# Optimization experiments

Measured on AMD Instinct MI355X. Metric: run time of the kernel, lower is better.

Reference implementation:

```python
import math
import numpy as np
import jax
import jax.numpy as jnp

RANK = 8
KITER = 2
EPS = 1e-5


def frft_time(z, alpha):
    # z: complex64 [B, T, C]; fractional Fourier transform along axis 1
    # via Bluestein-style chirp multiplication + FFT convolution.
    T = z.shape[1]
    a = (float(alpha) + math.pi) % (2.0 * math.pi) - math.pi
    if abs(a) < 1e-6:
        return z
    if abs(abs(a) - math.pi) < 1e-6:
        ph = np.complex64(np.exp(1j * math.copysign(math.pi / 2, a)))
        return ph * jnp.flip(z, axis=1)
    sa = math.sin(a)
    s = math.copysign(1.0 / max(1e-7, abs(sa)), sa)
    c = math.cos(a) / max(1e-7, sa)
    t = np.linspace(-1.0, 1.0, T)
    dt = 2.0 / (T - 1)
    tail = (1,) * (z.ndim - 2)
    pre = jnp.asarray(np.exp(1j * np.pi * (c + s) * t ** 2).astype(np.complex64)).reshape(1, T, *tail)
    g = z * pre
    m = np.arange(-(T - 1), T)
    L = 1 << (2 * T - 2).bit_length()  # next pow2 >= 2T-1
    h_pad = np.zeros(L, np.complex64)
    h_pad[m % L] = np.exp(-1j * np.pi * s * (m * dt) ** 2).astype(np.complex64)
    H = jnp.asarray(np.fft.fft(h_pad).astype(np.complex64)).reshape(1, L, *tail)
    pad = [(0, 0), (0, L - T)] + [(0, 0)] * (z.ndim - 2)
    G = jnp.fft.fft(jnp.pad(g, pad), axis=1)
    conv = jnp.fft.ifft(G * H, axis=1)[:, T - 1:T - 1 + T]
    pref = np.complex64(np.sqrt(np.complex64(1.0 - 1j * c)))
    return pref * pre * conv * np.float32(dt)


def _orthonorm(V):
    # batched reduced QR with deterministic column signs (sign of diag(R))
    Q, R = jnp.linalg.qr(V)
    d = jnp.diagonal(R, axis1=-2, axis2=-1)
    return Q * jnp.sign(d + EPS)[:, None, :]


def _forward(x, Win_shift, Wout_shift, b_shift, W_out, ln_gamma, ln_beta):
    B, T, D = x.shape
    anchor = jnp.zeros((B, D), x.dtype).at[:, 0].set(1.0)
    xc = x - anchor[:, None, :]
    # LowRankShift: S(x) = W_out_shift @ gelu(W_in_shift @ x) + b
    s = jax.nn.gelu(x @ Win_shift.T, approximate=False) @ Wout_shift.T + b_shift
    xprime = xc + s
    xpc = xprime.astype(jnp.complex64)
    alphas = np.linspace(0.15, 2.99, RANK)
    # per-alpha FrFT-domain energy weights
    weights = []
    for alpha in alphas:
        X_a = frft_time(xpc, alpha)
        E_a = jnp.mean(jnp.abs(X_a) ** 2, axis=2)  # [B,T]
        w_a = jnp.sqrt(E_a + 1e-6)  # pow p=0.5
        w_a = w_a / (jnp.mean(w_a, axis=1, keepdims=True) + 1e-6)
        weights.append((float(alpha), w_a))

    def Komega(Y):  # Y: real [B,T,r]
        Yc = Y.astype(jnp.complex64)
        acc = 0.0
        for alpha, w in weights:
            Ya = frft_time(Yc, alpha)
            acc = acc + frft_time(w[..., None].astype(jnp.complex64) * Ya, -alpha)
        return (acc / len(weights)).real

    # subspace iteration with identity init
    E0 = jnp.zeros((B, D, RANK), x.dtype).at[:, :RANK, :].set(jnp.eye(RANK, dtype=x.dtype))
    V = _orthonorm(E0)
    for _ in range(KITER):
        Y = Komega(xprime @ V)  # [B,T,r]
        Z = jnp.einsum('btd,btr->bdr', xprime, Y) / float(T)
        V = _orthonorm(Z + EPS * V)
    # sign-align columns to anchor
    sgn = jnp.sign(jnp.sum(V * anchor[:, :, None], axis=1) + 1e-12)
    V = V * sgn[:, None, :]
    traces = xprime @ V  # [B,T,r]
    scales = jnp.sqrt(jnp.sum(traces ** 2, axis=1, keepdims=True) + EPS)
    traces_n = traces / scales
    # shrink_lambda == 0 -> soft_shrink identity; SpiralMix(rank=1) has no pairs -> identity
    traces_final = traces_n * scales
    x_tilde = jnp.einsum('btr,bdr->btd', traces_final, V)
    x_hat = x_tilde - s + anchor[:, None, :]
    y = x + x_hat @ W_out.T  # dropout eval mode
    mu = jnp.mean(y, axis=-1, keepdims=True)
    var = jnp.mean((y - mu) ** 2, axis=-1, keepdims=True)
    return (y - mu) / jnp.sqrt(var + 1e-5) * ln_gamma + ln_beta


def setup_inputs():
    key = jax.random.key(0)
    k = jax.random.split(key, 5)
    B, T, D, SR = 4, 2048, 256, 128
    return {
        'x': jax.random.normal(k[0], (B, T, D), jnp.float32),
        'Win_shift': jax.random.normal(k[1], (SR, D), jnp.float32) / np.float32(np.sqrt(D)),
        'Wout_shift': jax.random.normal(k[2], (D, SR), jnp.float32) / np.float32(np.sqrt(SR)),
        'b_shift': jax.random.normal(k[3], (D,), jnp.float32) * 0.01,
        'W_out': jax.random.normal(k[4], (D, D), jnp.float32) / np.float32(np.sqrt(D)),
        'ln_gamma': jnp.ones((D,), jnp.float32),
        'ln_beta': jnp.zeros((D,), jnp.float32),
    }


def reference(x, Win_shift, Wout_shift, b_shift, W_out, ln_gamma, ln_beta):
    return _forward(x, Win_shift, Wout_shift, b_shift, W_out, ln_gamma, ln_beta)
```

## Files before the change

### kernel.cpp

```cpp
#include <hip/hip_runtime.h>
#include <math.h>

#define Bb 4
#define Tt 2048
#define Dd 256
#define SRr 128
#define Rr 8
#define NA 8
#define NV 16
#define Lf 4096
#define EPSf 1e-5f
#define PI_D 3.14159265358979323846

#define OFF_TW4R  0
#define OFF_TW4I  (OFF_TW4R + 4096)
#define OFF_PRER  (OFF_TW4I + 4096)
#define OFF_PREI  (OFF_PRER + NV*Tt)
#define OFF_POSR  (OFF_PREI + NV*Tt)
#define OFF_POSI  (OFF_POSR + NV*Tt)
#define OFF_PM2   (OFF_POSI + NV*Tt)
#define OFF_H     (OFF_PM2 + NA*Tt)
#define OFF_WINT  (OFF_H + NV*Lf*2)
#define OFF_WOUTT (OFF_WINT + Dd*SRr)
#define OFF_WOT   (OFF_WOUTT + SRr*Dd)
#define OFF_WTAB  (OFF_WOT + Dd*Dd)
#define OFF_ESUM  (OFF_WTAB + NA*Bb*Tt)
#define OFF_V     (OFF_ESUM + NA*Bb*Tt)
#define OFF_M     (OFF_V + Bb*Dd*Rr)
#define OFF_YT    (OFF_M + Bb*Dd*Rr)
#define OFF_YACC  (OFF_YT + Bb*Rr*Tt)
#define OFF_S     (OFF_YACC + Bb*Rr*Tt)
#define OFF_XPT   (OFF_S + Bb*Tt*Dd)

__device__ __forceinline__ float block_reduce_sum(float v, float* red, int tid){
  #pragma unroll
  for (int o = 32; o > 0; o >>= 1) v += __shfl_xor(v, o, 64);
  __syncthreads();
  if ((tid & 63) == 0) red[tid >> 6] = v;
  __syncthreads();
  return red[0] + red[1] + red[2] + red[3];
}

__device__ void variant_params(int v, double& s_, double& c_){
  double step = (2.99 - 0.15) / 7.0;
  int idx = v & 7;
  double alpha = (idx == 7) ? 2.99 : (0.15 + (double)idx * step);
  if (v >= 8) alpha = -alpha;
  double a = fmod(alpha + PI_D, 2.0 * PI_D);
  if (a < 0.0) a += 2.0 * PI_D;
  a -= PI_D;
  double sa = sin(a);
  s_ = ((sa >= 0.0) ? 1.0 : -1.0) / fmax(1e-7, fabs(sa));
  c_ = cos(a) / fmax(1e-7, sa);
}

struct cpx { float r, i; };
__device__ __forceinline__ cpx cmul(cpx a, cpx b){ return {a.r*b.r - a.i*b.i, a.r*b.i + a.i*b.r}; }
__device__ __forceinline__ cpx cmulj(cpx a, cpx b){ return {a.r*b.r + a.i*b.i, a.i*b.r - a.r*b.i}; }

__device__ __forceinline__ void fft4(cpx& a, cpx& b, cpx& c, cpx& d, float sgn){
  cpx t0{a.r+c.r, a.i+c.i}, t1{a.r-c.r, a.i-c.i};
  cpx t2{b.r+d.r, b.i+d.i}, t3{b.r-d.r, b.i-d.i};
  a = {t0.r+t2.r, t0.i+t2.i};
  c = {t0.r-t2.r, t0.i-t2.i};
  b = {t1.r - sgn*t3.i, t1.i + sgn*t3.r};
  d = {t1.r + sgn*t3.i, t1.i - sgn*t3.r};
}

__device__ __forceinline__ void fft16(cpx x[16], float sgn){
  const float WC[10] = {1.f, 0.92387953251128674f, 0.70710678118654752f, 0.38268343236508977f,
                        0.f, -0.38268343236508977f, -0.70710678118654752f, -0.92387953251128674f,
                        -1.f, -0.92387953251128674f};
  const float WS[10] = {0.f, 0.38268343236508977f, 0.70710678118654752f, 0.92387953251128674f,
                        1.f, 0.92387953251128674f, 0.70710678118654752f, 0.38268343236508977f,
                        0.f, -0.38268343236508977f};
  #pragma unroll
  for (int j0 = 0; j0 < 4; ++j0)
    fft4(x[j0], x[j0+4], x[j0+8], x[j0+12], sgn);
  #pragma unroll
  for (int j0 = 1; j0 < 4; ++j0){
    #pragma unroll
    for (int p0 = 1; p0 < 4; ++p0){
      int m = j0*p0;
      cpx w{WC[m], sgn*WS[m]};
      x[j0 + 4*p0] = cmul(x[j0 + 4*p0], w);
    }
  }
  #pragma unroll
  for (int p0 = 0; p0 < 4; ++p0)
    fft4(x[4*p0+0], x[4*p0+1], x[4*p0+2], x[4*p0+3], sgn);
  cpx t;
  t=x[1];  x[1]=x[4];   x[4]=t;
  t=x[2];  x[2]=x[8];   x[8]=t;
  t=x[3];  x[3]=x[12];  x[12]=t;
  t=x[6];  x[6]=x[9];   x[9]=t;
  t=x[7];  x[7]=x[13];  x[13]=t;
  t=x[11]; x[11]=x[14]; x[14]=t;
}

__device__ __forceinline__ void fft4096(cpx x[16], float* sre, float* sim,
                                        const cpx twA[16], const cpx twB[16],
                                        int tid, float sgn){
  int hi = tid >> 4, lo = tid & 15;
  fft16(x, sgn);
  #pragma unroll
  for (int p = 1; p < 16; ++p) x[p] = (sgn < 0.f) ? cmul(x[p], twA[p]) : cmulj(x[p], twA[p]);
  __syncthreads();
  #pragma unroll
  for (int p = 0; p < 16; ++p){ int a = p*272 + 17*hi + lo; sre[a] = x[p].r; sim[a] = x[p].i; }
  __syncthreads();
  #pragma unroll
  for (int u = 0; u < 16; ++u){ int a = hi*272 + 17*u + lo; x[u] = {sre[a], sim[a]}; }
  fft16(x, sgn);
  #pragma unroll
  for (int q = 1; q < 16; ++q) x[q] = (sgn < 0.f) ? cmul(x[q], twB[q]) : cmulj(x[q], twB[q]);
  __syncthreads();
  #pragma unroll
  for (int q = 0; q < 16; ++q){ int a = hi*272 + 17*q + lo; sre[a] = x[q].r; sim[a] = x[q].i; }
  __syncthreads();
  #pragma unroll
  for (int v = 0; v < 16; ++v){ int a = hi*272 + 17*lo + v; x[v] = {sre[a], sim[a]}; }
  fft16(x, sgn);
}

__global__ void k_twiddle(float* ws){
  int id = blockIdx.x*256 + threadIdx.x;
  for (int k = id; k < 4096; k += 4096){
    double ang = -2.0 * PI_D * (double)k / (double)Lf;
    ws[OFF_TW4R + k] = (float)cos(ang);
    ws[OFF_TW4I + k] = (float)sin(ang);
  }
}

__global__ void k_tables(float* ws){
  int v = blockIdx.x;
  double s_, c_;
  variant_params(v, s_, c_);
  double dt = 2.0 / (double)(Tt - 1);
  double cf = (double)(float)c_;
  double rmag = sqrt(1.0 + cf * cf);
  double pr = sqrt((rmag + 1.0) * 0.5);
  double pim = ((cf >= 0.0) ? -1.0 : 1.0) * sqrt(fmax(0.0, (rmag - 1.0) * 0.5));
  double cps = PI_D * (c_ + s_);
  double sc = dt / (double)Lf;
  for (int k = threadIdx.x; k < Tt; k += 256){
    double t = (k == Tt - 1) ? 1.0 : ((double)k * dt - 1.0);
    double th = cps * (t * t);
    double cr = cos(th), ci = sin(th);
    ws[OFF_PRER + v*Tt + k] = (float)cr;
    ws[OFF_PREI + v*Tt + k] = (float)ci;
    float por = (float)((pr*cr - pim*ci) * sc);
    float poi = (float)((pr*ci + pim*cr) * sc);
    ws[OFF_POSR + v*Tt + k] = por;
    ws[OFF_POSI + v*Tt + k] = poi;
    if (v < NA) ws[OFF_PM2 + v*Tt + k] = por*por + poi*poi;
  }
}

__global__ __launch_bounds__(256) void k_hfft(float* ws){
  __shared__ float sre[16*272], sim[16*272];
  int v = blockIdx.x, tid = threadIdx.x;
  int hi = tid >> 4, lo = tid & 15;
  int base = hi + 16*lo;
  double s_, c_;
  variant_params(v, s_, c_);
  double dt = 2.0 / (double)(Tt - 1);
  double ns = -(PI_D * s_);
  const float* tw4r = ws + OFF_TW4R; const float* tw4i = ws + OFF_TW4I;
  cpx twA[16], twB[16];
  #pragma unroll
  for (int p = 0; p < 16; ++p){
    int iA = tid * p;      twA[p] = {tw4r[iA], tw4i[iA]};
    int iB = 16 * lo * p;  twB[p] = {tw4r[iB], tw4i[iB]};
  }
  cpx x[16];
  #pragma unroll
  for (int j = 0; j < 16; ++j){
    int n = j*256 + tid;
    if (n == 2048){ x[j] = {0.f, 0.f}; continue; }
    int m = (n <= 2047) ? n : (n - 4096);
    double md = (double)m * dt;
    double th = ns * (md * md);
    x[j] = {(float)cos(th), (float)sin(th)};
  }
  fft4096(x, sre, sim, twA, twB, tid, -1.f);
  #pragma unroll
  for (int r = 0; r < 16; ++r){
    int k = base + 256*r;
    ws[OFF_H + (v*Lf + k)*2 + 0] = x[r].r;
    ws[OFF_H + (v*Lf + k)*2 + 1] = x[r].i;
  }
}

__global__ void k_transpose(const float* Win, const float* Wout, const float* Wo, float* ws){
  int id = blockIdx.x * 256 + threadIdx.x;
  { int d = id & (Dd-1); int k = id >> 8; ws[OFF_WOT + id] = Wo[d*Dd + k]; }
  if (id < Dd*SRr){
    int c = id & (SRr-1); int k = id >> 7;
    ws[OFF_WINT + id] = Win[c*Dd + k];
    int d2 = id & (Dd-1); int k2 = id >> 8;
    ws[OFF_WOUTT + id] = Wout[d2*SRr + k2];
  }
}

__global__ __launch_bounds__(256) void k_shift(const float* x, const float* bsh, float* ws){
  __shared__ float xs[16][Dd];
  __shared__ float us[16][SRr];
  int tid = threadIdx.x;
  int g0 = blockIdx.x * 16;
  int b = g0 >> 11, t0 = g0 & (Tt - 1);
  #pragma unroll
  for (int row = 0; row < 16; ++row)
    xs[row][tid] = x[(g0 + row)*Dd + tid];
  __syncthreads();
  int col = tid & 127, rowgrp = tid >> 7;
  {
    float acc[8];
    #pragma unroll
    for (int rr = 0; rr < 8; ++rr) acc[rr] = 0.f;
    const float* WT = ws + OFF_WINT;
    for (int k = 0; k < Dd; ++k){
      float w = WT[k*SRr + col];
      #pragma unroll
      for (int rr = 0; rr < 8; ++rr)
        acc[rr] = fmaf(xs[rowgrp*8 + rr][k], w, acc[rr]);
    }
    #pragma unroll
    for (int rr = 0; rr < 8; ++rr){
      float a = acc[rr];
      us[rowgrp*8 + rr][col] = 0.5f * a * (1.0f + erff(a * 0.70710678118654752f));
    }
  }
  __syncthreads();
  float sacc[16];
  float bv = bsh[tid];
  #pragma unroll
  for (int row = 0; row < 16; ++row) sacc[row] = bv;
  const float* WT2 = ws + OFF_WOUTT;
  for (int k = 0; k < SRr; ++k){
    float w = WT2[k*Dd + tid];
    #pragma unroll
    for (int row = 0; row < 16; ++row)
      sacc[row] = fmaf(us[row][k], w, sacc[row]);
  }
  float xp[16];
  #pragma unroll
  for (int row = 0; row < 16; ++row){
    float xv = xs[row][tid];
    float anc = (tid == 0) ? 1.0f : 0.0f;
    ws[OFF_S + (g0 + row)*Dd + tid] = sacc[row];
    xp[row] = xv - anc + sacc[row];
  }
  float* xpt = ws + OFF_XPT + (b*Dd + tid)*Tt + t0;
  #pragma unroll
  for (int q = 0; q < 4; ++q)
    *reinterpret_cast<float4*>(xpt + 4*q) = make_float4(xp[4*q], xp[4*q+1], xp[4*q+2], xp[4*q+3]);
}

__global__ __launch_bounds__(256) void k_weights(float* ws){
  __shared__ float sre[16*272], sim[16*272];
  int tid = threadIdx.x;
  int chunk = blockIdx.x, b = blockIdx.y, z = blockIdx.z;
  int hi = tid >> 4, lo = tid & 15;
  int base = hi + 16*lo;
  const float* tw4r = ws + OFF_TW4R; const float* tw4i = ws + OFF_TW4I;
  cpx twA[16], twB[16];
  #pragma unroll
  for (int p = 0; p < 16; ++p){
    int iA = tid * p;      twA[p] = {tw4r[iA], tw4i[iA]};
    int iB = 16 * lo * p;  twB[p] = {tw4r[iB], tw4i[iB]};
  }
  const float* prer = ws + OFF_PRER + z*Tt;
  const float* prei = ws + OFF_PREI + z*Tt;
  const float* pm2  = ws + OFF_PM2  + z*Tt;
  const float* Hv   = ws + OFF_H    + z*Lf*2;
  float e[16];
  #pragma unroll
  for (int r = 0; r < 16; ++r) e[r] = 0.f;
  for (int cc = 0; cc < 8; ++cc){
    int c = chunk*8 + cc;
    const float* xcol = ws + OFF_XPT + (b*Dd + c)*Tt;
    cpx x[16];
    #pragma unroll
    for (int j = 0; j < 16; ++j){
      if (j < 8){
        int t = j*256 + tid;
        float xv = xcol[t];
        x[j] = {xv * prer[t], xv * prei[t]};
      } else x[j] = {0.f, 0.f};
    }
    fft4096(x, sre, sim, twA, twB, tid, -1.f);
    #pragma unroll
    for (int r = 0; r < 16; ++r){
      int k = base + 256*r;
      cpx h{Hv[2*k], Hv[2*k+1]};
      x[r] = cmul(x[r], h);
    }
    __syncthreads();
    #pragma unroll
    for (int r = 0; r < 16; ++r){ int a = r*272 + 17*lo + hi; sre[a] = x[r].r; sim[a] = x[r].i; }
    __syncthreads();
    #pragma unroll
    for (int j = 0; j < 16; ++j){ int a = j*272 + 17*hi + lo; x[j] = {sre[a], sim[a]}; }
    fft4096(x, sre, sim, twA, twB, tid, +1.f);
    #pragma unroll
    for (int r = 0; r < 16; ++r){
      int k = base + 256*r;
      if (k >= 2047 && k < 4095){
        int t = k - 2047;
        e[r] += pm2[t] * (x[r].r*x[r].r + x[r].i*x[r].i);
      }
    }
  }
  float* Ez = ws + OFF_ESUM + (z*Bb + b)*Tt;
  #pragma unroll
  for (int r = 0; r < 16; ++r){
    int k = base + 256*r;
    if (k >= 2047 && k < 4095) atomicAdd(&Ez[k - 2047], e[r]);
  }
}

__global__ void k_wnorm(float* ws){
  __shared__ float red[4];
  int b = blockIdx.x, z = blockIdx.y, tid = threadIdx.x;
  const float* Ez = ws + OFF_ESUM + (z*Bb + b)*Tt;
  float* wz = ws + OFF_WTAB + (z*Bb + b)*Tt;
  float wr[8]; float psum = 0.f;
  #pragma unroll
  for (int k = 0; k < 8; ++k){
    float Ea = Ez[tid + k*256] * (1.0f / (float)Dd);
    wr[k] = sqrtf(Ea + 1e-6f);
    psum += wr[k];
  }
  float tot = block_reduce_sum(psum, red, tid);
  float inv = 1.0f / (tot / (float)Tt + 1e-6f);
  #pragma unroll
  for (int k = 0; k < 8; ++k) wz[tid + k*256] = wr[k] * inv;
}

__global__ void k_vinit(float* ws){
  int id = blockIdx.x*256 + threadIdx.x;
  int r = id & (Rr-1); int d = (id >> 3) & (Dd-1);
  ws[OFF_V + id] = (d == r) ? 1.f : 0.f;
}

__global__ void k_traces(float* ws){
  __shared__ float Vl[Dd*Rr];
  int tile = blockIdx.x, b = blockIdx.y, tid = threadIdx.x;
  for (int i = tid; i < Dd*Rr; i += 256) Vl[i] = ws[OFF_V + b*Dd*Rr + i];
  __syncthreads();
  int t = tile*256 + tid;
  float acc[Rr];
  #pragma unroll
  for (int r = 0; r < Rr; ++r) acc[r] = 0.f;
  const float* xp = ws + OFF_XPT + (b*Dd)*Tt + t;
  for (int d = 0; d < Dd; ++d){
    float xv = xp[d*Tt];
    #pragma unroll
    for (int r = 0; r < Rr; ++r) acc[r] = fmaf(xv, Vl[d*Rr + r], acc[r]);
  }
  #pragma unroll
  for (int r = 0; r < Rr; ++r) ws[OFF_YT + (b*Rr + r)*Tt + t] = acc[r];
}

__global__ __launch_bounds__(256) void k_komega(float* ws){
  __shared__ float sre[16*272], sim[16*272];
  int tid = threadIdx.x;
  int rr = blockIdx.x, b = blockIdx.y, z = blockIdx.z;
  int hi = tid >> 4, lo = tid & 15;
  int base = hi + 16*lo;
  int v1 = z, v2 = z + NA;
  const float* tw4r = ws + OFF_TW4R; const float* tw4i = ws + OFF_TW4I;
  cpx twA[16], twB[16];
  #pragma unroll
  for (int p = 0; p < 16; ++p){
    int iA = tid * p;      twA[p] = {tw4r[iA], tw4i[iA]};
    int iB = 16 * lo * p;  twB[p] = {tw4r[iB], tw4i[iB]};
  }
  const float* prer1 = ws + OFF_PRER + v1*Tt; const float* prei1 = ws + OFF_PREI + v1*Tt;
  const float* posr1 = ws + OFF_POSR + v1*Tt; const float* posi1 = ws + OFF_POSI + v1*Tt;
  const float* prer2 = ws + OFF_PRER + v2*Tt; const float* prei2 = ws + OFF_PREI + v2*Tt;
  const float* posr2 = ws + OFF_POSR + v2*Tt; const float* posi2 = ws + OFF_POSI + v2*Tt;
  const float* H1 = ws + OFF_H + v1*Lf*2;
  const float* H2 = ws + OFF_H + v2*Lf*2;
  const float* wz = ws + OFF_WTAB + (z*Bb + b)*Tt;
  const float* ycol = ws + OFF_YT + (b*Rr + rr)*Tt;
  float* yac = ws + OFF_YACC + (b*Rr + rr)*Tt;
  cpx x[16];
  #pragma unroll
  for (int j = 0; j < 16; ++j){
    if (j < 8){
      int t = j*256 + tid;
      float yv = ycol[t];
      x[j] = {yv * prer1[t], yv * prei1[t]};
    } else x[j] = {0.f, 0.f};
  }
  fft4096(x, sre, sim, twA, twB, tid, -1.f);
  #pragma unroll
  for (int r = 0; r < 16; ++r){ int k = base + 256*r; cpx h{H1[2*k], H1[2*k+1]}; x[r] = cmul(x[r], h); }
  __syncthreads();
  #pragma unroll
  for (int r = 0; r < 16; ++r){ int a = r*272 + 17*lo + hi; sre[a] = x[r].r; sim[a] = x[r].i; }
  __syncthreads();
  #pragma unroll
  for (int j = 0; j < 16; ++j){ int a = j*272 + 17*hi + lo; x[j] = {sre[a], sim[a]}; }
  fft4096(x, sre, sim, twA, twB, tid, +1.f);
  __syncthreads();
  #pragma unroll
  for (int r = 0; r < 16; ++r){
    int k = base + 256*r;
    if (k >= 2047 && k < 4095){
      int t = k - 2047;
      float cr = x[r].r, ci = x[r].i;
      float wv = wz[t];
      float yar = (posr1[t]*cr - posi1[t]*ci) * wv;
      float yai = (posr1[t]*ci + posi1[t]*cr) * wv;
      float gr = yar*prer2[t] - yai*prei2[t];
      float gi = yar*prei2[t] + yai*prer2[t];
      int a = (t >> 8)*272 + 17*((t >> 4) & 15) + (t & 15);
      sre[a] = gr; sim[a] = gi;
    }
  }
  __syncthreads();
  #pragma unroll
  for (int j = 0; j < 16; ++j){
    if (j < 8){ int a = j*272 + 17*hi + lo; x[j] = {sre[a], sim[a]}; }
    else x[j] = {0.f, 0.f};
  }
  fft4096(x, sre, sim, twA, twB, tid, -1.f);
  #pragma unroll
  for (int r = 0; r < 16; ++r){ int k = base + 256*r; cpx h{H2[2*k], H2[2*k+1]}; x[r] = cmul(x[r], h); }
  __syncthreads();
  #pragma unroll
  for (int r = 0; r < 16; ++r){ int a = r*272 + 17*lo + hi; sre[a] = x[r].r; sim[a] = x[r].i; }
  __syncthreads();
  #pragma unroll
  for (int j = 0; j < 16; ++j){ int a = j*272 + 17*hi + lo; x[j] = {sre[a], sim[a]}; }
  fft4096(x, sre, sim, twA, twB, tid, +1.f);
  #pragma unroll
  for (int r = 0; r < 16; ++r){
    int k = base + 256*r;
    if (k >= 2047 && k < 4095){
      int t = k - 2047;
      atomicAdd(&yac[t], posr2[t]*x[r].r - posi2[t]*x[r].i);
    }
  }
}

__global__ void k_zm(float* ws){
  __shared__ float red[4];
  int d = blockIdx.x, b = blockIdx.y, tid = threadIdx.x;
  const float* xcol = ws + OFF_XPT + (b*Dd + d)*Tt;
  for (int r = 0; r < Rr; ++r){
    const float* ycol = ws + OFF_YACC + (b*Rr + r)*Tt;
    float p = 0.f;
    for (int t = tid; t < Tt; t += 256) p = fmaf(xcol[t], ycol[t], p);
    float tot = block_reduce_sum(p, red, tid);
    if (tid == 0){
      float zval = tot / (float)(Tt * NA);
      ws[OFF_M + (b*Dd + d)*Rr + r] = zval + EPSf * ws[OFF_V + (b*Dd + d)*Rr + r];
    }
  }
}

__global__ void k_mgs(float* ws){
  __shared__ float q[Rr][Dd];
  __shared__ float red[4];
  int b = blockIdx.x, tid = threadIdx.x;
  float m[Rr];
  #pragma unroll
  for (int r = 0; r < Rr; ++r) m[r] = ws[OFF_M + (b*Dd + tid)*Rr + r];
  for (int r = 0; r < Rr; ++r){
    float v = m[r];
    for (int j = 0; j < r; ++j){
      float dotv = block_reduce_sum(q[j][tid] * v, red, tid);
      v = fmaf(-dotv, q[j][tid], v);
    }
    float n2 = block_reduce_sum(v * v, red, tid);
    q[r][tid] = v / sqrtf(n2);
    __syncthreads();
  }
  #pragma unroll
  for (int r = 0; r < Rr; ++r) ws[OFF_V + (b*Dd + tid)*Rr + r] = q[r][tid];
}

__global__ __launch_bounds__(256) void k_out(const float* x, const float* g, const float* be,
                                             float* ws, float* out){
  __shared__ float hs[16][Dd + 1];
  __shared__ float ytl[16][Rr];
  __shared__ float mv_mu[16], mv_rs[16];
  int tid = threadIdx.x;
  int g0 = blockIdx.x * 16;
  int b = g0 >> 11, t0 = g0 & (Tt - 1);
  if (tid < 128){
    int row = tid >> 3, r = tid & 7;
    ytl[row][r] = ws[OFF_YT + (b*Rr + r)*Tt + t0 + row];
  }
  float vr[Rr];
  {
    const float4* Vb = reinterpret_cast<const float4*>(ws + OFF_V + (b*Dd + tid)*Rr);
    float4 v0 = Vb[0], v1 = Vb[1];
    vr[0]=v0.x; vr[1]=v0.y; vr[2]=v0.z; vr[3]=v0.w;
    vr[4]=v1.x; vr[5]=v1.y; vr[6]=v1.z; vr[7]=v1.w;
  }
  __syncthreads();
  #pragma unroll
  for (int row = 0; row < 16; ++row){
    float acc = 0.f;
    #pragma unroll
    for (int r = 0; r < Rr; ++r) acc = fmaf(ytl[row][r], vr[r], acc);
    acc -= ws[OFF_S + (g0 + row)*Dd + tid];
    if (tid == 0) acc += 1.0f;
    hs[row][tid] = acc;
  }
  __syncthreads();
  float acc[16];
  #pragma unroll
  for (int row = 0; row < 16; ++row) acc[row] = x[(g0 + row)*Dd + tid];
  const float* WT = ws + OFF_WOT;
  for (int k = 0; k < Dd; ++k){
    float w = WT[k*Dd + tid];
    #pragma unroll
    for (int row = 0; row < 16; ++row)
      acc[row] = fmaf(hs[row][k], w, acc[row]);
  }
  __syncthreads();
  #pragma unroll
  for (int row = 0; row < 16; ++row) hs[row][tid] = acc[row];
  __syncthreads();
  {
    int row = tid >> 4, j = tid & 15;
    float yv[16]; float sum = 0.f;
    #pragma unroll
    for (int mth = 0; mth < 16; ++mth){ yv[mth] = hs[row][j + 16*mth]; sum += yv[mth]; }
    #pragma unroll
    for (int o = 8; o > 0; o >>= 1) sum += __shfl_xor(sum, o, 16);
    float mu = sum * (1.0f / (float)Dd);
    float ssq = 0.f;
    #pragma unroll
    for (int mth = 0; mth < 16; ++mth){ float d = yv[mth] - mu; ssq = fmaf(d, d, ssq); }
    #pragma unroll
    for (int o = 8; o > 0; o >>= 1) ssq += __shfl_xor(ssq, o, 16);
    if (j == 0){ mv_mu[row] = mu; mv_rs[row] = rsqrtf(ssq * (1.0f / (float)Dd) + 1e-5f); }
  }
  __syncthreads();
  float gg = g[tid], bb = be[tid];
  #pragma unroll
  for (int row = 0; row < 16; ++row)
    out[(g0 + row)*Dd + tid] = (acc[row] - mv_mu[row]) * mv_rs[row] * gg + bb;
}

extern "C" void kernel_launch(void* const* d_in, const int* in_sizes, int n_in,
                              void* d_out, int out_size, void* d_ws, size_t ws_size,
                              hipStream_t stream){
  (void)in_sizes; (void)n_in; (void)out_size; (void)ws_size;
  const float* x    = (const float*)d_in[0];
  const float* Win  = (const float*)d_in[1];
  const float* Wout = (const float*)d_in[2];
  const float* bsh  = (const float*)d_in[3];
  const float* Wo   = (const float*)d_in[4];
  const float* g    = (const float*)d_in[5];
  const float* be   = (const float*)d_in[6];
  float* ws  = (float*)d_ws;
  float* out = (float*)d_out;

  hipLaunchKernelGGL(k_twiddle, dim3(16), dim3(256), 0, stream, ws);
  hipLaunchKernelGGL(k_tables, dim3(NV), dim3(256), 0, stream, ws);
  hipLaunchKernelGGL(k_hfft, dim3(NV), dim3(256), 0, stream, ws);
  hipLaunchKernelGGL(k_transpose, dim3(Dd*Dd/256), dim3(256), 0, stream, Win, Wout, Wo, ws);
  hipLaunchKernelGGL(k_shift, dim3(Bb*Tt/16), dim3(256), 0, stream, x, bsh, ws);
  hipMemsetAsync(ws + OFF_ESUM, 0, (size_t)NA*Bb*Tt*sizeof(float), stream);
  hipLaunchKernelGGL(k_weights, dim3(Dd/8, Bb, NA), dim3(256), 0, stream, ws);
  hipLaunchKernelGGL(k_wnorm, dim3(Bb, NA), dim3(256), 0, stream, ws);
  hipLaunchKernelGGL(k_vinit, dim3(Bb*Dd*Rr/256), dim3(256), 0, stream, ws);
  for (int it = 0; it < 2; ++it){
    hipLaunchKernelGGL(k_traces, dim3(Tt/256, Bb), dim3(256), 0, stream, ws);
    hipMemsetAsync(ws + OFF_YACC, 0, (size_t)Bb*Rr*Tt*sizeof(float), stream);
    hipLaunchKernelGGL(k_komega, dim3(Rr, Bb, NA), dim3(256), 0, stream, ws);
    hipLaunchKernelGGL(k_zm, dim3(Dd, Bb), dim3(256), 0, stream, ws);
    hipLaunchKernelGGL(k_mgs, dim3(Bb), dim3(256), 0, stream, ws);
  }
  hipLaunchKernelGGL(k_traces, dim3(Tt/256, Bb), dim3(256), 0, stream, ws);
  hipLaunchKernelGGL(k_out, dim3(Bb*Tt/16), dim3(256), 0, stream, x, g, be, ws, out);
}
```

Before: 487.6 us.

## Merge setup kernels, skip zero-padded FFT stage, replace atomics with per-alpha buffers

```diff
diff --git a/kernel.cpp b/kernel.cpp
--- a/kernel.cpp
+++ b/kernel.cpp
@@ -28,8 +28,8 @@
 #define OFF_V     (OFF_ESUM + NA*Bb*Tt)
 #define OFF_M     (OFF_V + Bb*Dd*Rr)
 #define OFF_YT    (OFF_M + Bb*Dd*Rr)
-#define OFF_YACC  (OFF_YT + Bb*Rr*Tt)
-#define OFF_S     (OFF_YACC + Bb*Rr*Tt)
+#define OFF_YAC8  (OFF_YT + Bb*Rr*Tt)
+#define OFF_S     (OFF_YAC8 + NA*Bb*Rr*Tt)
 #define OFF_XPT   (OFF_S + Bb*Tt*Dd)
 
 __device__ __forceinline__ float block_reduce_sum(float v, float* red, int tid){
@@ -67,6 +67,7 @@
   d = {t1.r + sgn*t3.i, t1.i - sgn*t3.r};
 }
 
+template<int ZP>
 __device__ __forceinline__ void fft16(cpx x[16], float sgn){
   const float WC[10] = {1.f, 0.92387953251128674f, 0.70710678118654752f, 0.38268343236508977f,
                         0.f, -0.38268343236508977f, -0.70710678118654752f, -0.92387953251128674f,
@@ -74,9 +75,20 @@
   const float WS[10] = {0.f, 0.38268343236508977f, 0.70710678118654752f, 0.92387953251128674f,
                         1.f, 0.92387953251128674f, 0.70710678118654752f, 0.38268343236508977f,
                         0.f, -0.38268343236508977f};
-  #pragma unroll
-  for (int j0 = 0; j0 < 4; ++j0)
-    fft4(x[j0], x[j0+4], x[j0+8], x[j0+12], sgn);
+  if (ZP){
+    #pragma unroll
+    for (int j0 = 0; j0 < 4; ++j0){
+      cpx a = x[j0], b = x[j0+4];
+      x[j0]    = {a.r + b.r,       a.i + b.i};
+      x[j0+4]  = {a.r - sgn*b.i,   a.i + sgn*b.r};
+      x[j0+8]  = {a.r - b.r,       a.i - b.i};
+      x[j0+12] = {a.r + sgn*b.i,   a.i - sgn*b.r};
+    }
+  } else {
+    #pragma unroll
+    for (int j0 = 0; j0 < 4; ++j0)
+      fft4(x[j0], x[j0+4], x[j0+8], x[j0+12], sgn);
+  }
   #pragma unroll
   for (int j0 = 1; j0 < 4; ++j0){
     #pragma unroll
@@ -98,81 +110,85 @@
   t=x[11]; x[11]=x[14]; x[14]=t;
 }
 
-__device__ __forceinline__ void fft4096(cpx x[16], float* sre, float* sim,
-                                        const cpx twA[16], const cpx twB[16],
-                                        int tid, float sgn){
+template<int ZP>
+__device__ __forceinline__ void fft4096c(cpx x[16], float2* sh,
+                                         const cpx twA[16], const cpx twB[16],
+                                         int tid, float sgn){
   int hi = tid >> 4, lo = tid & 15;
-  fft16(x, sgn);
+  fft16<ZP>(x, sgn);
   #pragma unroll
   for (int p = 1; p < 16; ++p) x[p] = (sgn < 0.f) ? cmul(x[p], twA[p]) : cmulj(x[p], twA[p]);
   __syncthreads();
   #pragma unroll
-  for (int p = 0; p < 16; ++p){ int a = p*272 + 17*hi + lo; sre[a] = x[p].r; sim[a] = x[p].i; }
-  __syncthreads();
-  #pragma unroll
-  for (int u = 0; u < 16; ++u){ int a = hi*272 + 17*u + lo; x[u] = {sre[a], sim[a]}; }
-  fft16(x, sgn);
+  for (int p = 0; p < 16; ++p){ sh[p*272 + 17*hi + lo] = make_float2(x[p].r, x[p].i); }
+  __syncthreads();
+  #pragma unroll
+  for (int u = 0; u < 16; ++u){ float2 v = sh[hi*272 + 17*u + lo]; x[u] = {v.x, v.y}; }
+  fft16<0>(x, sgn);
   #pragma unroll
   for (int q = 1; q < 16; ++q) x[q] = (sgn < 0.f) ? cmul(x[q], twB[q]) : cmulj(x[q], twB[q]);
   __syncthreads();
   #pragma unroll
-  for (int q = 0; q < 16; ++q){ int a = hi*272 + 17*q + lo; sre[a] = x[q].r; sim[a] = x[q].i; }
-  __syncthreads();
-  #pragma unroll
-  for (int v = 0; v < 16; ++v){ int a = hi*272 + 17*lo + v; x[v] = {sre[a], sim[a]}; }
-  fft16(x, sgn);
-}
-
-__global__ void k_twiddle(float* ws){
-  int id = blockIdx.x*256 + threadIdx.x;
-  for (int k = id; k < 4096; k += 4096){
-    double ang = -2.0 * PI_D * (double)k / (double)Lf;
-    ws[OFF_TW4R + k] = (float)cos(ang);
-    ws[OFF_TW4I + k] = (float)sin(ang);
-  }
-}
-
-__global__ void k_tables(float* ws){
-  int v = blockIdx.x;
+  for (int q = 0; q < 16; ++q){ sh[hi*272 + 17*q + lo] = make_float2(x[q].r, x[q].i); }
+  __syncthreads();
+  #pragma unroll
+  for (int v = 0; v < 16; ++v){ float2 t = sh[hi*272 + 17*lo + v]; x[v] = {t.x, t.y}; }
+  fft16<0>(x, sgn);
+}
+
+__global__ __launch_bounds__(256) void k_setup(const float* Win, const float* Wout,
+                                               const float* Wo, float* ws){
+  __shared__ float2 sh[16*272];
+  int blk = blockIdx.x, tid = threadIdx.x;
+  int id = blk*256 + tid;
+  { int d = id & (Dd-1); int k = id >> 8; ws[OFF_WOT + id] = Wo[d*Dd + k]; }
+  if (id < Dd*SRr){
+    int c = id & (SRr-1); int k = id >> 7;
+    ws[OFF_WINT + id] = Win[c*Dd + k];
+    int d2 = id & (Dd-1); int k2 = id >> 8;
+    ws[OFF_WOUTT + id] = Wout[d2*SRr + k2];
+  }
+  if (id < 4096){
+    double ang = -2.0 * PI_D * (double)id / (double)Lf;
+    ws[OFF_TW4R + id] = (float)cos(ang);
+    ws[OFF_TW4I + id] = (float)sin(ang);
+  }
+  if (blk >= NV) return;
+  int v = blk;
   double s_, c_;
   variant_params(v, s_, c_);
   double dt = 2.0 / (double)(Tt - 1);
-  double cf = (double)(float)c_;
-  double rmag = sqrt(1.0 + cf * cf);
-  double pr = sqrt((rmag + 1.0) * 0.5);
-  double pim = ((cf >= 0.0) ? -1.0 : 1.0) * sqrt(fmax(0.0, (rmag - 1.0) * 0.5));
-  double cps = PI_D * (c_ + s_);
-  double sc = dt / (double)Lf;
-  for (int k = threadIdx.x; k < Tt; k += 256){
-    double t = (k == Tt - 1) ? 1.0 : ((double)k * dt - 1.0);
-    double th = cps * (t * t);
-    double cr = cos(th), ci = sin(th);
-    ws[OFF_PRER + v*Tt + k] = (float)cr;
-    ws[OFF_PREI + v*Tt + k] = (float)ci;
-    float por = (float)((pr*cr - pim*ci) * sc);
-    float poi = (float)((pr*ci + pim*cr) * sc);
-    ws[OFF_POSR + v*Tt + k] = por;
-    ws[OFF_POSI + v*Tt + k] = poi;
-    if (v < NA) ws[OFF_PM2 + v*Tt + k] = por*por + poi*poi;
-  }
-}
-
-__global__ __launch_bounds__(256) void k_hfft(float* ws){
-  __shared__ float sre[16*272], sim[16*272];
-  int v = blockIdx.x, tid = threadIdx.x;
+  {
+    double cf = (double)(float)c_;
+    double rmag = sqrt(1.0 + cf * cf);
+    double pr = sqrt((rmag + 1.0) * 0.5);
+    double pim = ((cf >= 0.0) ? -1.0 : 1.0) * sqrt(fmax(0.0, (rmag - 1.0) * 0.5));
+    double cps = PI_D * (c_ + s_);
+    double sc = dt / (double)Lf;
+    for (int k = tid; k < Tt; k += 256){
+      double t = (k == Tt - 1) ? 1.0 : ((double)k * dt - 1.0);
+      double th = cps * (t * t);
+      double cr = cos(th), ci = sin(th);
+      ws[OFF_PRER + v*Tt + k] = (float)cr;
+      ws[OFF_PREI + v*Tt + k] = (float)ci;
+      float por = (float)((pr*cr - pim*ci) * sc);
+      float poi = (float)((pr*ci + pim*cr) * sc);
+      ws[OFF_POSR + v*Tt + k] = por;
+      ws[OFF_POSI + v*Tt + k] = poi;
+      if (v < NA) ws[OFF_PM2 + v*Tt + k] = por*por + poi*poi;
+    }
+  }
   int hi = tid >> 4, lo = tid & 15;
   int base = hi + 16*lo;
-  double s_, c_;
-  variant_params(v, s_, c_);
-  double dt = 2.0 / (double)(Tt - 1);
+  cpx twA[16], twB[16];
+  #pragma unroll
+  for (int p = 0; p < 16; ++p){
+    double aA = -2.0 * PI_D * (double)((tid * p) & 4095) / (double)Lf;
+    double aB = -2.0 * PI_D * (double)((16 * lo * p) & 4095) / (double)Lf;
+    twA[p] = {(float)cos(aA), (float)sin(aA)};
+    twB[p] = {(float)cos(aB), (float)sin(aB)};
+  }
   double ns = -(PI_D * s_);
-  const float* tw4r = ws + OFF_TW4R; const float* tw4i = ws + OFF_TW4I;
-  cpx twA[16], twB[16];
-  #pragma unroll
-  for (int p = 0; p < 16; ++p){
-    int iA = tid * p;      twA[p] = {tw4r[iA], tw4i[iA]};
-    int iB = 16 * lo * p;  twB[p] = {tw4r[iB], tw4i[iB]};
-  }
   cpx x[16];
   #pragma unroll
   for (int j = 0; j < 16; ++j){
@@ -183,23 +199,12 @@
     double th = ns * (md * md);
     x[j] = {(float)cos(th), (float)sin(th)};
   }
-  fft4096(x, sre, sim, twA, twB, tid, -1.f);
+  fft4096c<0>(x, sh, twA, twB, tid, -1.f);
   #pragma unroll
   for (int r = 0; r < 16; ++r){
     int k = base + 256*r;
     ws[OFF_H + (v*Lf + k)*2 + 0] = x[r].r;
     ws[OFF_H + (v*Lf + k)*2 + 1] = x[r].i;
-  }
-}
-
-__global__ void k_transpose(const float* Win, const float* Wout, const float* Wo, float* ws){
-  int id = blockIdx.x * 256 + threadIdx.x;
-  { int d = id & (Dd-1); int k = id >> 8; ws[OFF_WOT + id] = Wo[d*Dd + k]; }
-  if (id < Dd*SRr){
-    int c = id & (SRr-1); int k = id >> 7;
-    ws[OFF_WINT + id] = Win[c*Dd + k];
-    int d2 = id & (Dd-1); int k2 = id >> 8;
-    ws[OFF_WOUTT + id] = Wout[d2*SRr + k2];
   }
 }
 
@@ -251,14 +256,14 @@
     ws[OFF_S + (g0 + row)*Dd + tid] = sacc[row];
     xp[row] = xv - anc + sacc[row];
   }
-  float* xpt = ws + OFF_XPT + (b*Dd + tid)*Tt + t0;
+  float* xpt = ws + OFF_XPT + ((size_t)(b*Dd + tid))*Tt + t0;
   #pragma unroll
   for (int q = 0; q < 4; ++q)
     *reinterpret_cast<float4*>(xpt + 4*q) = make_float4(xp[4*q], xp[4*q+1], xp[4*q+2], xp[4*q+3]);
 }
 
-__global__ __launch_bounds__(256) void k_weights(float* ws){
-  __shared__ float sre[16*272], sim[16*272];
+__global__ __launch_bounds__(256, 4) void k_weights(float* ws){
+  __shared__ float2 sh[16*272];
   int tid = threadIdx.x;
   int chunk = blockIdx.x, b = blockIdx.y, z = blockIdx.z;
   int hi = tid >> 4, lo = tid & 15;
@@ -279,17 +284,17 @@
   for (int r = 0; r < 16; ++r) e[r] = 0.f;
   for (int cc = 0; cc < 8; ++cc){
     int c = chunk*8 + cc;
-    const float* xcol = ws + OFF_XPT + (b*Dd + c)*Tt;
+    const float* xcol = ws + OFF_XPT + ((size_t)(b*Dd + c))*Tt;
     cpx x[16];
     #pragma unroll
-    for (int j = 0; j < 16; ++j){
-      if (j < 8){
-        int t = j*256 + tid;
-        float xv = xcol[t];
-        x[j] = {xv * prer[t], xv * prei[t]};
-      } else x[j] = {0.f, 0.f};
-    }
-    fft4096(x, sre, sim, twA, twB, tid, -1.f);
+    for (int j = 0; j < 8; ++j){
+      int t = j*256 + tid;
+      float xv = xcol[t];
+      x[j] = {xv * prer[t], xv * prei[t]};
+    }
+    #pragma unroll
+    for (int j = 8; j < 16; ++j) x[j] = {0.f, 0.f};
+    fft4096c<1>(x, sh, twA, twB, tid, -1.f);
     #pragma unroll
     for (int r = 0; r < 16; ++r){
       int k = base + 256*r;
@@ -298,11 +303,11 @@
     }
     __syncthreads();
     #pragma unroll
-    for (int r = 0; r < 16; ++r){ int a = r*272 + 17*lo + hi; sre[a] = x[r].r; sim[a] = x[r].i; }
+    for (int r = 0; r < 16; ++r){ sh[r*272 + 17*lo + hi] = make_float2(x[r].r, x[r].i); }
     __syncthreads();
     #pragma unroll
-    for (int j = 0; j < 16; ++j){ int a = j*272 + 17*hi + lo; x[j] = {sre[a], sim[a]}; }
-    fft4096(x, sre, sim, twA, twB, tid, +1.f);
+    for (int j = 0; j < 16; ++j){ float2 v = sh[j*272 + 17*hi + lo]; x[j] = {v.x, v.y}; }
+    fft4096c<0>(x, sh, twA, twB, tid, +1.f);
     #pragma unroll
     for (int r = 0; r < 16; ++r){
       int k = base + 256*r;
@@ -338,12 +343,6 @@
   for (int k = 0; k < 8; ++k) wz[tid + k*256] = wr[k] * inv;
 }
 
-__global__ void k_vinit(float* ws){
-  int id = blockIdx.x*256 + threadIdx.x;
-  int r = id & (Rr-1); int d = (id >> 3) & (Dd-1);
-  ws[OFF_V + id] = (d == r) ? 1.f : 0.f;
-}
-
 __global__ void k_traces(float* ws){
   __shared__ float Vl[Dd*Rr];
   int tile = blockIdx.x, b = blockIdx.y, tid = threadIdx.x;
@@ -353,9 +352,9 @@
   float acc[Rr];
   #pragma unroll
   for (int r = 0; r < Rr; ++r) acc[r] = 0.f;
-  const float* xp = ws + OFF_XPT + (b*Dd)*Tt + t;
+  const float* xp = ws + OFF_XPT + ((size_t)(b*Dd))*Tt + t;
   for (int d = 0; d < Dd; ++d){
-    float xv = xp[d*Tt];
+    float xv = xp[(size_t)d*Tt];
     #pragma unroll
     for (int r = 0; r < Rr; ++r) acc[r] = fmaf(xv, Vl[d*Rr + r], acc[r]);
   }
@@ -363,8 +362,8 @@
   for (int r = 0; r < Rr; ++r) ws[OFF_YT + (b*Rr + r)*Tt + t] = acc[r];
 }
 
-__global__ __launch_bounds__(256) void k_komega(float* ws){
-  __shared__ float sre[16*272], sim[16*272];
+__global__ __launch_bounds__(256, 4) void k_komega(float* ws, int useXPT){
+  __shared__ float2 sh[16*272];
   int tid = threadIdx.x;
   int rr = blockIdx.x, b = blockIdx.y, z = blockIdx.z;
   int hi = tid >> 4, lo = tid & 15;
@@ -384,27 +383,28 @@
   const float* H1 = ws + OFF_H + v1*Lf*2;
   const float* H2 = ws + OFF_H + v2*Lf*2;
   const float* wz = ws + OFF_WTAB + (z*Bb + b)*Tt;
-  const float* ycol = ws + OFF_YT + (b*Rr + rr)*Tt;
-  float* yac = ws + OFF_YACC + (b*Rr + rr)*Tt;
+  const float* ycol = useXPT ? (ws + OFF_XPT + ((size_t)(b*Dd + rr))*Tt)
+                             : (ws + OFF_YT + ((size_t)(b*Rr + rr))*Tt);
+  float* yac = ws + OFF_YAC8 + ((size_t)((z*Bb + b)*Rr + rr))*Tt;
   cpx x[16];
   #pragma unroll
-  for (int j = 0; j < 16; ++j){
-    if (j < 8){
-      int t = j*256 + tid;
-      float yv = ycol[t];
-      x[j] = {yv * prer1[t], yv * prei1[t]};
-    } else x[j] = {0.f, 0.f};
-  }
-  fft4096(x, sre, sim, twA, twB, tid, -1.f);
+  for (int j = 0; j < 8; ++j){
+    int t = j*256 + tid;
+    float yv = ycol[t];
+    x[j] = {yv * prer1[t], yv * prei1[t]};
+  }
+  #pragma unroll
+  for (int j = 8; j < 16; ++j) x[j] = {0.f, 0.f};
+  fft4096c<1>(x, sh, twA, twB, tid, -1.f);
   #pragma unroll
   for (int r = 0; r < 16; ++r){ int k = base + 256*r; cpx h{H1[2*k], H1[2*k+1]}; x[r] = cmul(x[r], h); }
   __syncthreads();
   #pragma unroll
-  for (int r = 0; r < 16; ++r){ int a = r*272 + 17*lo + hi; sre[a] = x[r].r; sim[a] = x[r].i; }
-  __syncthreads();
-  #pragma unroll
-  for (int j = 0; j < 16; ++j){ int a = j*272 + 17*hi + lo; x[j] = {sre[a], sim[a]}; }
-  fft4096(x, sre, sim, twA, twB, tid, +1.f);
+  for (int r = 0; r < 16; ++r){ sh[r*272 + 17*lo + hi] = make_float2(x[r].r, x[r].i); }
+  __syncthreads();
+  #pragma unroll
+  for (int j = 0; j < 16; ++j){ float2 v = sh[j*272 + 17*hi + lo]; x[j] = {v.x, v.y}; }
+  fft4096c<0>(x, sh, twA, twB, tid, +1.f);
   __syncthreads();
   #pragma unroll
   for (int r = 0; r < 16; ++r){
@@ -418,47 +418,58 @@
       float gr = yar*prer2[t] - yai*prei2[t];
       float gi = yar*prei2[t] + yai*prer2[t];
       int a = (t >> 8)*272 + 17*((t >> 4) & 15) + (t & 15);
-      sre[a] = gr; sim[a] = gi;
-    }
-  }
-  __syncthreads();
-  #pragma unroll
-  for (int j = 0; j < 16; ++j){
-    if (j < 8){ int a = j*272 + 17*hi + lo; x[j] = {sre[a], sim[a]}; }
-    else x[j] = {0.f, 0.f};
-  }
-  fft4096(x, sre, sim, twA, twB, tid, -1.f);
+      sh[a] = make_float2(gr, gi);
+    }
+  }
+  __syncthreads();
+  #pragma unroll
+  for (int j = 0; j < 8; ++j){ float2 v = sh[j*272 + 17*hi + lo]; x[j] = {v.x, v.y}; }
+  #pragma unroll
+  for (int j = 8; j < 16; ++j) x[j] = {0.f, 0.f};
+  fft4096c<1>(x, sh, twA, twB, tid, -1.f);
   #pragma unroll
   for (int r = 0; r < 16; ++r){ int k = base + 256*r; cpx h{H2[2*k], H2[2*k+1]}; x[r] = cmul(x[r], h); }
   __syncthreads();
   #pragma unroll
-  for (int r = 0; r < 16; ++r){ int a = r*272 + 17*lo + hi; sre[a] = x[r].r; sim[a] = x[r].i; }
-  __syncthreads();
-  #pragma unroll
-  for (int j = 0; j < 16; ++j){ int a = j*272 + 17*hi + lo; x[j] = {sre[a], sim[a]}; }
-  fft4096(x, sre, sim, twA, twB, tid, +1.f);
+  for (int r = 0; r < 16; ++r){ sh[r*272 + 17*lo + hi] = make_float2(x[r].r, x[r].i); }
+  __syncthreads();
+  #pragma unroll
+  for (int j = 0; j < 16; ++j){ float2 v = sh[j*272 + 17*hi + lo]; x[j] = {v.x, v.y}; }
+  fft4096c<0>(x, sh, twA, twB, tid, +1.f);
   #pragma unroll
   for (int r = 0; r < 16; ++r){
     int k = base + 256*r;
     if (k >= 2047 && k < 4095){
       int t = k - 2047;
-      atomicAdd(&yac[t], posr2[t]*x[r].r - posi2[t]*x[r].i);
-    }
-  }
-}
-
-__global__ void k_zm(float* ws){
+      yac[t] = posr2[t]*x[r].r - posi2[t]*x[r].i;
+    }
+  }
+}
+
+__global__ void k_ysum(float* ws){
+  int i = (blockIdx.x*256 + threadIdx.x) * 4;
+  float4 acc = make_float4(0.f, 0.f, 0.f, 0.f);
+  #pragma unroll
+  for (int z = 0; z < NA; ++z){
+    float4 v = *reinterpret_cast<const float4*>(ws + OFF_YAC8 + (size_t)z*Bb*Rr*Tt + i);
+    acc.x += v.x; acc.y += v.y; acc.z += v.z; acc.w += v.w;
+  }
+  *reinterpret_cast<float4*>(ws + OFF_YT + i) = acc;
+}
+
+__global__ void k_zm(float* ws, int useIdent){
   __shared__ float red[4];
   int d = blockIdx.x, b = blockIdx.y, tid = threadIdx.x;
-  const float* xcol = ws + OFF_XPT + (b*Dd + d)*Tt;
+  const float* xcol = ws + OFF_XPT + ((size_t)(b*Dd + d))*Tt;
   for (int r = 0; r < Rr; ++r){
-    const float* ycol = ws + OFF_YACC + (b*Rr + r)*Tt;
+    const float* ycol = ws + OFF_YT + (b*Rr + r)*Tt;
     float p = 0.f;
     for (int t = tid; t < Tt; t += 256) p = fmaf(xcol[t], ycol[t], p);
     float tot = block_reduce_sum(p, red, tid);
     if (tid == 0){
       float zval = tot / (float)(Tt * NA);
-      ws[OFF_M + (b*Dd + d)*Rr + r] = zval + EPSf * ws[OFF_V + (b*Dd + d)*Rr + r];
+      float vprev = useIdent ? ((d == r) ? 1.f : 0.f) : ws[OFF_V + (b*Dd + d)*Rr + r];
+      ws[OFF_M + (b*Dd + d)*Rr + r] = zval + EPSf * vprev;
     }
   }
 }
@@ -564,22 +575,20 @@
   float* ws  = (float*)d_ws;
   float* out = (float*)d_out;
 
-  hipLaunchKernelGGL(k_twiddle, dim3(16), dim3(256), 0, stream, ws);
-  hipLaunchKernelGGL(k_tables, dim3(NV), dim3(256), 0, stream, ws);
-  hipLaunchKernelGGL(k_hfft, dim3(NV), dim3(256), 0, stream, ws);
-  hipLaunchKernelGGL(k_transpose, dim3(Dd*Dd/256), dim3(256), 0, stream, Win, Wout, Wo, ws);
+  hipLaunchKernelGGL(k_setup, dim3(256), dim3(256), 0, stream, Win, Wout, Wo, ws);
   hipLaunchKernelGGL(k_shift, dim3(Bb*Tt/16), dim3(256), 0, stream, x, bsh, ws);
   hipMemsetAsync(ws + OFF_ESUM, 0, (size_t)NA*Bb*Tt*sizeof(float), stream);
   hipLaunchKernelGGL(k_weights, dim3(Dd/8, Bb, NA), dim3(256), 0, stream, ws);
   hipLaunchKernelGGL(k_wnorm, dim3(Bb, NA), dim3(256), 0, stream, ws);
-  hipLaunchKernelGGL(k_vinit, dim3(Bb*Dd*Rr/256), dim3(256), 0, stream, ws);
-  for (int it = 0; it < 2; ++it){
-    hipLaunchKernelGGL(k_traces, dim3(Tt/256, Bb), dim3(256), 0, stream, ws);
-    hipMemsetAsync(ws + OFF_YACC, 0, (size_t)Bb*Rr*Tt*sizeof(float), stream);
-    hipLaunchKernelGGL(k_komega, dim3(Rr, Bb, NA), dim3(256), 0, stream, ws);
-    hipLaunchKernelGGL(k_zm, dim3(Dd, Bb), dim3(256), 0, stream, ws);
-    hipLaunchKernelGGL(k_mgs, dim3(Bb), dim3(256), 0, stream, ws);
-  }
+  hipLaunchKernelGGL(k_komega, dim3(Rr, Bb, NA), dim3(256), 0, stream, ws, 1);
+  hipLaunchKernelGGL(k_ysum, dim3(64), dim3(256), 0, stream, ws);
+  hipLaunchKernelGGL(k_zm, dim3(Dd, Bb), dim3(256), 0, stream, ws, 1);
+  hipLaunchKernelGGL(k_mgs, dim3(Bb), dim3(256), 0, stream, ws);
+  hipLaunchKernelGGL(k_traces, dim3(Tt/256, Bb), dim3(256), 0, stream, ws);
+  hipLaunchKernelGGL(k_komega, dim3(Rr, Bb, NA), dim3(256), 0, stream, ws, 0);
+  hipLaunchKernelGGL(k_ysum, dim3(64), dim3(256), 0, stream, ws);
+  hipLaunchKernelGGL(k_zm, dim3(Dd, Bb), dim3(256), 0, stream, ws, 0);
+  hipLaunchKernelGGL(k_mgs, dim3(Bb), dim3(256), 0, stream, ws);
   hipLaunchKernelGGL(k_traces, dim3(Tt/256, Bb), dim3(256), 0, stream, ws);
   hipLaunchKernelGGL(k_out, dim3(Bb*Tt/16), dim3(256), 0, stream, x, g, be, ws, out);
 }
```

New measurement: 624.1 us. 28.0% more time.
